# Performance work log

Measured on AMD Instinct MI355X. Metric: run time of the kernel, lower is better.

The kernel has to match this reference:

```python
import jax, jax.numpy as jnp
import numpy as np

EPS = 1e-12

def _layernorm(x, gamma, beta):
    m = jnp.mean(x, axis=-1, keepdims=True)
    v = jnp.mean((x - m) ** 2, axis=-1, keepdims=True)
    return (x - m) * jax.lax.rsqrt(v + EPS) * gamma + beta

def _gcn(x, node_emb, time_emb, W_pool, b_pool, gamma, beta):
    # x: [B, N, C]; node_emb: [N, D]; time_emb: [D]
    e = _layernorm(node_emb + time_emb[None, :], gamma, beta)          # [N, D] (dropout off: eval mode)
    A = jax.nn.softmax(e @ e.T, axis=1)                                 # [N, N] dynamic adjacency
    weights = jnp.einsum('nd,dkio->nkio', e, W_pool)                    # [N, 2, C, O] node-adaptive weights
    bias = e @ b_pool                                                   # [N, O]
    # supports = [I, A]; I support is identity -> x itself
    x_g = jnp.stack([x, jnp.einsum('nm,bmc->bnc', A, x)], axis=2)       # [B, N, 2, C]
    return jnp.einsum('bnki,nkio->bno', x_g, weights) + bias            # [B, N, O]

def setup_inputs() -> dict:
    key = jax.random.key(0)
    ks = jax.random.split(key, 16)
    B, N, Din, H, D = 64, 2048, 2, 64, 16
    C = Din + H
    inp = {
        'x': jax.random.normal(ks[0], (B, N, Din), jnp.float32),
        'state': jax.random.normal(ks[1], (B, N, H), jnp.float32),
        'node_embeddings': jax.random.normal(ks[2], (N, D), jnp.float32),
        'time_embeddings': jax.random.normal(ks[3], (D,), jnp.float32),
    }
    for i, g in enumerate(['z', 'r', 'u']):
        inp[f'W_{g}'] = jax.random.normal(ks[4 + 2 * i], (D, 2, C, H), jnp.float32) * 0.02
        inp[f'b_{g}'] = jax.random.normal(ks[5 + 2 * i], (D, H), jnp.float32) * 0.02
        inp[f'gamma_{g}'] = jnp.ones((D,), jnp.float32)
        inp[f'beta_{g}'] = jnp.zeros((D,), jnp.float32)
    return inp

def reference(x, state, node_embeddings, time_embeddings,
              W_z, b_z, gamma_z, beta_z,
              W_r, b_r, gamma_r, beta_r,
              W_u, b_u, gamma_u, beta_u):
    xs = jnp.concatenate([x, state], axis=-1)                           # [B, N, Din+H]
    z = jax.nn.sigmoid(_gcn(xs, node_embeddings, time_embeddings, W_z, b_z, gamma_z, beta_z))
    r = jax.nn.sigmoid(_gcn(xs, node_embeddings, time_embeddings, W_r, b_r, gamma_r, beta_r))
    cand = jnp.concatenate([x, z * state], axis=-1)
    hc = jnp.tanh(_gcn(cand, node_embeddings, time_embeddings, W_u, b_u, gamma_u, beta_u))
    return r * state + (1.0 - r) * hc
```

## Files before the change

kernel.cpp:

```cpp
#include <hip/hip_runtime.h>
#include <hip/hip_bf16.h>
#include <math.h>


typedef __attribute__((ext_vector_type(4))) float f4;
typedef __attribute__((ext_vector_type(8))) short s8;

#define B_   64
#define N_   2048
#define DIN  2
#define H_   64
#define D_   16
#define C_   66
#define KI   132
#define KIP  160
#define CB   4224

#define GLD16(gp, lp) __builtin_amdgcn_global_load_lds((const __attribute__((address_space(1))) void*)(gp), (__attribute__((address_space(3))) void*)(lp), 16, 0, 0)

static __device__ __forceinline__ ushort f2bf(float v) {
  __hip_bfloat16 h = __float2bfloat16(v);
  return *(ushort*)&h;
}
static __device__ __forceinline__ float bf2f(ushort u) {
  __hip_bfloat16 h = *(__hip_bfloat16*)&u;
  return __bfloat162float(h);
}
static __device__ __forceinline__ uint packbf(float a, float b) {
  return ((uint)f2bf(b) << 16) | f2bf(a);
}

__global__ void k_e(const float* __restrict__ node, const float* __restrict__ timee,
                    const float* __restrict__ g0, const float* __restrict__ b0,
                    const float* __restrict__ g1, const float* __restrict__ b1,
                    const float* __restrict__ g2, const float* __restrict__ b2,
                    float* __restrict__ e, ushort* __restrict__ ebf) {
  int n = blockIdx.x * blockDim.x + threadIdx.x;
  if (n >= N_) return;
  float v[D_]; float m = 0.f;
  #pragma unroll
  for (int d = 0; d < D_; ++d) { v[d] = node[n * D_ + d] + timee[d]; m += v[d]; }
  m *= (1.0f / D_);
  float var = 0.f;
  #pragma unroll
  for (int d = 0; d < D_; ++d) { float t = v[d] - m; var += t * t; }
  var *= (1.0f / D_);
  float r = rsqrtf(var + 1e-12f);
  float y[D_];
  #pragma unroll
  for (int d = 0; d < D_; ++d) y[d] = (v[d] - m) * r;
  const float* gs[3] = {g0, g1, g2};
  const float* bs[3] = {b0, b1, b2};
  #pragma unroll
  for (int g = 0; g < 3; ++g) {
    #pragma unroll
    for (int d = 0; d < D_; d += 2) {
      float o0 = y[d] * gs[g][d] + bs[g][d];
      float o1 = y[d + 1] * gs[g][d + 1] + bs[g][d + 1];
      e[g * N_ * D_ + n * D_ + d] = o0;
      e[g * N_ * D_ + n * D_ + d + 1] = o1;
      *(uint*)&ebf[g * N_ * D_ + n * D_ + d] = packbf(o0, o1);
    }
  }
}

__global__ __launch_bounds__(256)
void k_attn(const ushort* __restrict__ ebf, __hip_bfloat16* __restrict__ A) {
  __shared__ __align__(16) ushort eb[N_ * D_];
  __shared__ float red[4][16];
  const int t = threadIdx.x;
  const ushort* eg = ebf + (size_t)blockIdx.z * (N_ * D_);
  {
    const uint4* src = (const uint4*)eg;
    uint4* dst = (uint4*)eb;
    #pragma unroll
    for (int i = 0; i < 16; ++i) dst[i * 256 + t] = src[i * 256 + t];
  }
  __syncthreads();
  const int lane = t & 63, w = t >> 6;
  const int l15 = lane & 15, q = lane >> 4;
  const int r0 = blockIdx.x * 16;
  s8 rf = {0, 0, 0, 0, 0, 0, 0, 0};
  if (q < 2) rf = *(const s8*)&eb[(r0 + l15) * D_ + q * 8];
  const int c0 = w * 512;
  f4 acc[32];
  #pragma unroll
  for (int tl = 0; tl < 32; ++tl) {
    s8 cf = {0, 0, 0, 0, 0, 0, 0, 0};
    if (q < 2) cf = *(const s8*)&eb[(c0 + tl * 16 + l15) * D_ + q * 8];
    acc[tl] = __builtin_amdgcn_mfma_f32_16x16x32_bf16(cf, rf, (f4)0.0f, 0, 0, 0);
  }
  float m = acc[0][0];
  #pragma unroll
  for (int tl = 0; tl < 32; ++tl) {
    #pragma unroll
    for (int rg = 0; rg < 4; ++rg) m = fmaxf(m, acc[tl][rg]);
  }
  m = fmaxf(m, __shfl_xor(m, 16, 64));
  m = fmaxf(m, __shfl_xor(m, 32, 64));
  if (lane < 16) red[w][l15] = m;
  __syncthreads();
  const float gm = fmaxf(fmaxf(red[0][l15], red[1][l15]), fmaxf(red[2][l15], red[3][l15]));
  __syncthreads();
  float ps = 0.f;
  #pragma unroll
  for (int tl = 0; tl < 32; ++tl) {
    #pragma unroll
    for (int rg = 0; rg < 4; ++rg) {
      float v = __expf(acc[tl][rg] - gm);
      acc[tl][rg] = v;
      ps += v;
    }
  }
  ps += __shfl_xor(ps, 16, 64);
  ps += __shfl_xor(ps, 32, 64);
  if (lane < 16) red[w][l15] = ps;
  __syncthreads();
  const float inv = 1.0f / (red[0][l15] + red[1][l15] + red[2][l15] + red[3][l15]);
  ushort* Ar = (ushort*)A + (size_t)blockIdx.z * ((size_t)N_ * N_) +
               (size_t)(r0 + l15) * N_ + c0 + q * 4;
  #pragma unroll
  for (int tl = 0; tl < 32; ++tl) {
    uint2 pk;
    pk.x = packbf(acc[tl][0] * inv, acc[tl][1] * inv);
    pk.y = packbf(acc[tl][2] * inv, acc[tl][3] * inv);
    *(uint2*)&Ar[tl * 16] = pk;
  }
}

template <int MODE>
__global__ __launch_bounds__(256)
void k_buildX(const float* __restrict__ x, const float* __restrict__ state,
              const __hip_bfloat16* __restrict__ zbuf, __hip_bfloat16* __restrict__ XT) {
  constexpr int LDM = 72;
  __shared__ __align__(16) ushort T[C_ * LDM];
  const int t = threadIdx.x;
  const int m0 = blockIdx.x * 64, b = blockIdx.y;
  const int m = t >> 2, hq = t & 3;
  {
    const float* sp = state + ((size_t)b * N_ + m0 + m) * H_ + hq * 16;
    float sv[16];
    #pragma unroll
    for (int i = 0; i < 16; i += 4) {
      float4 v = *(const float4*)(sp + i);
      sv[i] = v.x; sv[i + 1] = v.y; sv[i + 2] = v.z; sv[i + 3] = v.w;
    }
    if (MODE) {
      const ushort* zp = (const ushort*)zbuf + ((size_t)b * N_ + m0 + m) * H_ + hq * 16;
      uint4 z0 = *(const uint4*)&zp[0], z1 = *(const uint4*)&zp[8];
      uint zw[8] = {z0.x, z0.y, z0.z, z0.w, z1.x, z1.y, z1.z, z1.w};
      #pragma unroll
      for (int i = 0; i < 8; ++i) {
        sv[2 * i]     *= bf2f((ushort)(zw[i] & 0xffffu));
        sv[2 * i + 1] *= bf2f((ushort)(zw[i] >> 16));
      }
    }
    #pragma unroll
    for (int i = 0; i < 16; ++i) T[(DIN + hq * 16 + i) * LDM + m] = f2bf(sv[i]);
    if (t < 64) {
      const float2 xv = *(const float2*)&x[((size_t)b * N_ + m0 + t) * DIN];
      T[0 * LDM + t] = f2bf(xv.x);
      T[1 * LDM + t] = f2bf(xv.y);
    }
  }
  __syncthreads();
  {
    int r = t >> 2, ch = t & 3;
    ushort* dst = (ushort*)XT + (size_t)(b * C_ + r) * N_ + m0 + ch * 16;
    *(uint4*)&dst[0] = *(uint4*)&T[r * LDM + ch * 16];
    *(uint4*)&dst[8] = *(uint4*)&T[r * LDM + ch * 16 + 8];
    if (t < 8) {
      r = 64 + (t >> 2);
      ushort* dst2 = (ushort*)XT + (size_t)(b * C_ + r) * N_ + m0 + ch * 16;
      *(uint4*)&dst2[0] = *(uint4*)&T[r * LDM + ch * 16];
      *(uint4*)&dst2[8] = *(uint4*)&T[r * LDM + ch * 16 + 8];
    }
  }
}

__global__ __launch_bounds__(256)
void k_gemm(const __hip_bfloat16* __restrict__ Abase, size_t astride,
            const __hip_bfloat16* __restrict__ XT,
            __hip_bfloat16* __restrict__ Ybase, size_t ystride) {
  __shared__ __align__(16) ushort At[2][128 * 32];
  __shared__ __align__(16) ushort Xt[2][128 * 32];
  const int t = threadIdx.x;
  const int nwg = gridDim.x * gridDim.y * gridDim.z;
  const int orig = blockIdx.x + gridDim.x * (blockIdx.y + gridDim.y * blockIdx.z);
  const int chunk = nwg >> 3;
  const int swz = (orig & 7) * chunk + (orig >> 3);
  const int bx = swz % gridDim.x;
  const int rest = swz / gridDim.x;
  const int by = rest % gridDim.y;
  const int bz = rest / gridDim.y;
  const int j0 = bx * 128, r0 = by * 128;
  const ushort* Ag = (const ushort*)Abase + (size_t)bz * astride;
  ushort* Y = (ushort*)Ybase + (size_t)bz * ystride;
  const int lane = t & 63, w = t >> 6;
  const int rowa = w * 32 + (lane >> 2);
  const int kc = (((lane & 3) ^ ((lane >> 3) & 3)) * 8);
  const ushort* pA0 = Ag + (size_t)(r0 + rowa) * N_ + kc;
  const ushort* pA1 = pA0 + 16 * N_;
  const ushort* pX0 = (const ushort*)XT + (size_t)(j0 + rowa) * N_ + kc;
  const ushort* pX1 = pX0 + 16 * N_;
  const int l15 = t & 15, q = (t >> 4) & 3;
  const int qs = (q ^ ((l15 >> 1) & 3)) * 8;
  const int wr = (w >> 1) * 64, wc = (w & 1) * 64;
  f4 acc[4][4];
  #pragma unroll
  for (int i = 0; i < 4; ++i)
    #pragma unroll
    for (int jj = 0; jj < 4; ++jj) acc[i][jj] = (f4)0.0f;
  GLD16(pA0, &At[0][(w * 32) * 32]);
  GLD16(pA1, &At[0][(w * 32 + 16) * 32]);
  GLD16(pX0, &Xt[0][(w * 32) * 32]);
  GLD16(pX1, &Xt[0][(w * 32 + 16) * 32]);
  pA0 += 32; pA1 += 32; pX0 += 32; pX1 += 32;
  int cur = 0;
  for (int k0 = 0; k0 < N_; k0 += 32) {
    if (k0 + 32 < N_) {
      const int nx = cur ^ 1;
      GLD16(pA0, &At[nx][(w * 32) * 32]);
      GLD16(pA1, &At[nx][(w * 32 + 16) * 32]);
      GLD16(pX0, &Xt[nx][(w * 32) * 32]);
      GLD16(pX1, &Xt[nx][(w * 32 + 16) * 32]);
      pA0 += 32; pA1 += 32; pX0 += 32; pX1 += 32;
      asm volatile("s_waitcnt vmcnt(4)" ::: "memory");
    } else {
      asm volatile("s_waitcnt vmcnt(0)" ::: "memory");
    }
    __builtin_amdgcn_s_barrier();
    __builtin_amdgcn_sched_barrier(0);
    s8 af[4], bfr[4];
    #pragma unroll
    for (int mi = 0; mi < 4; ++mi)
      af[mi] = *(const s8*)&At[cur][(wr + mi * 16 + l15) * 32 + qs];
    #pragma unroll
    for (int ni = 0; ni < 4; ++ni)
      bfr[ni] = *(const s8*)&Xt[cur][(wc + ni * 16 + l15) * 32 + qs];
    __builtin_amdgcn_s_setprio(1);
    #pragma unroll
    for (int mi = 0; mi < 4; ++mi)
      #pragma unroll
      for (int ni = 0; ni < 4; ++ni)
        acc[mi][ni] = __builtin_amdgcn_mfma_f32_16x16x32_bf16(af[mi], bfr[ni], acc[mi][ni], 0, 0, 0);
    __builtin_amdgcn_s_setprio(0);
    __builtin_amdgcn_s_barrier();
    cur ^= 1;
  }
  #pragma unroll
  for (int mi = 0; mi < 4; ++mi) {
    int rr = r0 + wr + mi * 16 + q * 4;
    #pragma unroll
    for (int ni = 0; ni < 4; ++ni) {
      int cc = j0 + wc + ni * 16 + l15;
      #pragma unroll
      for (int rg = 0; rg < 4; ++rg)
        Y[(size_t)(rr + rg) * CB + cc] = f2bf(acc[mi][ni][rg]);
    }
  }
}

__global__ __launch_bounds__(256)
void k_wmat(const float* __restrict__ eg, const float* __restrict__ Wp, ushort* __restrict__ Wm) {
  constexpr int TRS = 36;
  __shared__ float Wl[16 * 8 * 64];
  __shared__ ushort Tr[8 * 64 * TRS];
  const int t = threadIdx.x;
  const int n0 = blockIdx.x * 8;
  const int y = blockIdx.y;
  const int o = t & 63, w = t >> 6;
  const int ng = w & 1, krh = (w >> 1) * 4;
  float er[4][16];
  #pragma unroll
  for (int j = 0; j < 4; ++j) {
    const float* ep = eg + (size_t)(n0 + ng * 4 + j) * D_;
    #pragma unroll
    for (int d = 0; d < D_; d += 4) {
      float4 v = *(const float4*)(ep + d);
      er[j][d] = v.x; er[j][d + 1] = v.y; er[j][d + 2] = v.z; er[j][d + 3] = v.w;
    }
  }
  const int ngroups = (y == 3) ? 2 : 1;
  for (int g = 0; g < ngroups; ++g) {
    const int kic0 = y * 4 + g * 4;
    for (int kk = 0; kk < 4; ++kk) {
      const int kic = kic0 + kk;
      __syncthreads();
      #pragma unroll
      for (int it = 0; it < 8; ++it) {
        int f = it * 256 + t;
        int d = f >> 7, rem = f & 127, kr = rem >> 4, o4 = rem & 15;
        int ki = kic * 8 + kr;
        float4 v;
        if (ki < KI) v = *(const float4*)&Wp[((size_t)d * KI + ki) * 64 + o4 * 4];
        else { v.x = 0.f; v.y = 0.f; v.z = 0.f; v.w = 0.f; }
        *(float4*)&Wl[f * 4] = v;
      }
      __syncthreads();
      float a[4][4];
      #pragma unroll
      for (int j = 0; j < 4; ++j)
        #pragma unroll
        for (int k = 0; k < 4; ++k) a[j][k] = 0.f;
      for (int d = 0; d < D_; ++d) {
        float w4[4];
        #pragma unroll
        for (int k = 0; k < 4; ++k) w4[k] = Wl[(d * 8 + krh + k) * 64 + o];
        #pragma unroll
        for (int j = 0; j < 4; ++j)
          #pragma unroll
          for (int k = 0; k < 4; ++k) a[j][k] = fmaf(er[j][d], w4[k], a[j][k]);
      }
      #pragma unroll
      for (int j = 0; j < 4; ++j) {
        ushort* tr = &Tr[((ng * 4 + j) * 64 + o) * TRS + kk * 8 + krh];
        *(uint*)&tr[0] = packbf(a[j][0], a[j][1]);
        *(uint*)&tr[2] = packbf(a[j][2], a[j][3]);
      }
    }
    __syncthreads();
    const int k0 = kic0 * 8;
    #pragma unroll
    for (int p = 0; p < 8; ++p) {
      int u = p * 256 + t;
      int nl = u >> 8, oo = (u >> 2) & 63, qq = u & 3;
      const ushort* tr = &Tr[(nl * 64 + oo) * TRS + qq * 8];
      uint2 lo = *(const uint2*)&tr[0];
      uint2 hi = *(const uint2*)&tr[4];
      uint4 vv; vv.x = lo.x; vv.y = lo.y; vv.z = hi.x; vv.w = hi.y;
      *(uint4*)&Wm[((size_t)(n0 + nl) * 64 + oo) * KIP + k0 + qq * 8] = vv;
    }
  }
}

template <int MODE>
__global__ __launch_bounds__(256)
void k_einsum(const float* __restrict__ e, const ushort* __restrict__ Wm, const float* __restrict__ bp,
              const __hip_bfloat16* __restrict__ Y,
              const float* __restrict__ x, const float* __restrict__ state,
              const __hip_bfloat16* __restrict__ zbuf, const __hip_bfloat16* __restrict__ rbuf,
              void* __restrict__ outp) {
  constexpr int LDK = 168;
  constexpr int LDR = 72;
  __shared__ __align__(16) ushort xg[64 * LDK];
  __shared__ __align__(16) ushort res[64 * LDR];
  __shared__ float el[D_];
  __shared__ float bl[64];
  const int n = blockIdx.x, t = threadIdx.x;
  if (t < D_) el[t] = e[n * D_ + t];
  __syncthreads();
  if (t < 64) {
    float s = 0.f;
    #pragma unroll
    for (int d = 0; d < D_; ++d) s += el[d] * bp[d * 64 + t];
    bl[t] = s;
  }
  {
    const int b = t >> 2, j = t & 3;
    const size_t bn = (size_t)b * N_ + n;
    float sv[16];
    const float* sp = state + bn * 64 + j * 16;
    #pragma unroll
    for (int i = 0; i < 16; i += 4) {
      float4 v = *(const float4*)(sp + i);
      sv[i] = v.x; sv[i + 1] = v.y; sv[i + 2] = v.z; sv[i + 3] = v.w;
    }
    if (MODE) {
      const ushort* zp = (const ushort*)zbuf + bn * 64 + j * 16;
      uint4 z0 = *(const uint4*)&zp[0], z1 = *(const uint4*)&zp[8];
      uint zw[8] = {z0.x, z0.y, z0.z, z0.w, z1.x, z1.y, z1.z, z1.w};
      #pragma unroll
      for (int i = 0; i < 8; ++i) {
        sv[2 * i]     *= bf2f((ushort)(zw[i] & 0xffffu));
        sv[2 * i + 1] *= bf2f((ushort)(zw[i] >> 16));
      }
    }
    ushort* xr = &xg[b * LDK + 2 + j * 16];
    #pragma unroll
    for (int i = 0; i < 16; i += 2) {
      uint pk = packbf(sv[i], sv[i + 1]);
      *(uint*)&xr[i] = pk;
    }
    const ushort* yp = (const ushort*)Y + (size_t)n * CB + b * C_ + j * 16;
    uint* xy = (uint*)&xg[b * LDK + 66 + j * 16];
    #pragma unroll
    for (int i = 0; i < 8; ++i) xy[i] = *(const uint*)&yp[2 * i];
    if (j == 0) *(uint*)&xg[b * LDK + 130] = *(const uint*)&yp[64];
    if (t < 64) {
      const float* xp = x + ((size_t)t * N_ + n) * DIN;
      uint pk = packbf(xp[0], xp[1]);
      *(uint*)&xg[t * LDK] = pk;
    }
    ushort* pg = &xg[b * LDK + 132 + j * 7];
    #pragma unroll
    for (int i = 0; i < 7; ++i) pg[i] = 0;
  }
  __syncthreads();
  const int l15 = t & 15, q = (t >> 4) & 3, w = t >> 6;
  const int wm = (w >> 1) * 32, wn = (w & 1) * 32;
  const ushort* Wn = Wm + (size_t)n * (64 * KIP);
  f4 acc[2][2];
  acc[0][0] = acc[0][1] = acc[1][0] = acc[1][1] = (f4)0.0f;
  #pragma unroll
  for (int kk = 0; kk < KIP; kk += 32) {
    s8 af[2], bfr[2];
    #pragma unroll
    for (int mi = 0; mi < 2; ++mi) af[mi] = *(const s8*)&xg[(wm + mi * 16 + l15) * LDK + kk + q * 8];
    #pragma unroll
    for (int ni = 0; ni < 2; ++ni) bfr[ni] = *(const s8*)(Wn + (size_t)(wn + ni * 16 + l15) * KIP + kk + q * 8);
    #pragma unroll
    for (int mi = 0; mi < 2; ++mi)
      #pragma unroll
      for (int ni = 0; ni < 2; ++ni)
        acc[mi][ni] = __builtin_amdgcn_mfma_f32_16x16x32_bf16(af[mi], bfr[ni], acc[mi][ni], 0, 0, 0);
  }
  {
    float bl0 = bl[wn + l15], bl1 = bl[wn + 16 + l15];
    #pragma unroll
    for (int mi = 0; mi < 2; ++mi)
      #pragma unroll
      for (int ni = 0; ni < 2; ++ni) {
        float bb = ni ? bl1 : bl0;
        #pragma unroll
        for (int rg = 0; rg < 4; ++rg) {
          float v = acc[mi][ni][rg] + bb;
          float a;
          if (MODE == 0) a = 1.0f / (1.0f + __expf(-v));
          else           a = 1.0f - 2.0f / (__expf(2.0f * v) + 1.0f);
          res[(wm + mi * 16 + q * 4 + rg) * LDR + (wn + ni * 16 + l15)] = f2bf(a);
        }
      }
  }
  __syncthreads();
  {
    const int b = t >> 2, j = t & 3;
    const size_t gb = ((size_t)b * N_ + n) * 64 + j * 16;
    const ushort* rr = &res[b * LDR + j * 16];
    if (MODE == 0) {
      uint4 v0 = *(const uint4*)&rr[0];
      uint4 v1 = *(const uint4*)&rr[8];
      *(uint4*)((ushort*)outp + gb) = v0;
      *(uint4*)((ushort*)outp + gb + 8) = v1;
    } else {
      float* ob = (float*)outp;
      const float* stp = state + gb;
      const ushort* rp = (const ushort*)rbuf + gb;
      uint4 r0 = *(const uint4*)&rp[0], r1 = *(const uint4*)&rp[8];
      uint rw[8] = {r0.x, r0.y, r0.z, r0.w, r1.x, r1.y, r1.z, r1.w};
      #pragma unroll
      for (int i = 0; i < 16; i += 4) {
        float4 st = *(const float4*)(stp + i);
        float4 ov;
        float rv0 = bf2f((ushort)(rw[i / 2] & 0xffffu));
        float rv1 = bf2f((ushort)(rw[i / 2] >> 16));
        float rv2 = bf2f((ushort)(rw[i / 2 + 1] & 0xffffu));
        float rv3 = bf2f((ushort)(rw[i / 2 + 1] >> 16));
        ov.x = rv0 * st.x + (1.0f - rv0) * bf2f(rr[i]);
        ov.y = rv1 * st.y + (1.0f - rv1) * bf2f(rr[i + 1]);
        ov.z = rv2 * st.z + (1.0f - rv2) * bf2f(rr[i + 2]);
        ov.w = rv3 * st.w + (1.0f - rv3) * bf2f(rr[i + 3]);
        *(float4*)(ob + gb + i) = ov;
      }
    }
  }
}

extern "C" void kernel_launch(void* const* d_in, const int* in_sizes, int n_in,
                              void* d_out, int out_size, void* d_ws, size_t ws_size,
                              hipStream_t stream) {
  const float* x     = (const float*)d_in[0];
  const float* state = (const float*)d_in[1];
  const float* node  = (const float*)d_in[2];
  const float* timee = (const float*)d_in[3];
  const float* W_z = (const float*)d_in[4];
  const float* b_z = (const float*)d_in[5];
  const float* g_z = (const float*)d_in[6];
  const float* be_z = (const float*)d_in[7];
  const float* W_r = (const float*)d_in[8];
  const float* b_r = (const float*)d_in[9];
  const float* g_r = (const float*)d_in[10];
  const float* be_r = (const float*)d_in[11];
  const float* W_u = (const float*)d_in[12];
  const float* b_u = (const float*)d_in[13];
  const float* g_u = (const float*)d_in[14];
  const float* be_u = (const float*)d_in[15];

  constexpr size_t NN = (size_t)N_ * N_;
  constexpr size_t ND = (size_t)N_ * D_;
  char* ws = (char*)d_ws;
  float*           e  = (float*)(ws);
  __hip_bfloat16*  A  = (__hip_bfloat16*)(ws + 393216);
  __hip_bfloat16*  XT = (__hip_bfloat16*)(ws + 25559040);
  __hip_bfloat16*  Y  = (__hip_bfloat16*)(ws + 42860544);
  __hip_bfloat16*  zb = (__hip_bfloat16*)(ws + 60162048);
  __hip_bfloat16*  rb = (__hip_bfloat16*)(ws + 76939264);
  ushort*          ebf = (ushort*)(ws + 93716480);
  ushort*          Wm = (ushort*)(ws + 93716480);
  __hip_bfloat16*  Yr = (__hip_bfloat16*)(ws + 135659520);
  const size_t YRD = ((size_t)135659520 - 42860544) / 2;
  const bool big = ws_size >= (size_t)152961024;

  float* out = (float*)d_out;

  k_e<<<8, 256, 0, stream>>>(node, timee, g_z, be_z, g_r, be_r, g_u, be_u, e, ebf);
  k_attn<<<dim3(N_ / 16, 1, 3), 256, 0, stream>>>(ebf, A);
  k_buildX<0><<<dim3(32, 64), 256, 0, stream>>>(x, state, nullptr, XT);

  dim3 ggrid1(CB / 128, N_ / 128, 1);
  dim3 ggrid2(CB / 128, N_ / 128, 2);
  dim3 wgrid(N_ / 8, 4);

  if (big) {
    k_wmat<<<wgrid, 256, 0, stream>>>(e + 0 * ND, W_z, Wm);
    k_gemm<<<ggrid2, 256, 0, stream>>>(A, NN, XT, Y, YRD);
    k_einsum<0><<<N_, 256, 0, stream>>>(e + 0 * ND, Wm, b_z, Y, x, state, nullptr, nullptr, (void*)zb);
    k_wmat<<<wgrid, 256, 0, stream>>>(e + 1 * ND, W_r, Wm);
    k_einsum<0><<<N_, 256, 0, stream>>>(e + 1 * ND, Wm, b_r, Yr, x, state, nullptr, nullptr, (void*)rb);
  } else {
    k_wmat<<<wgrid, 256, 0, stream>>>(e + 0 * ND, W_z, Wm);
    k_gemm<<<ggrid1, 256, 0, stream>>>(A, 0, XT, Y, 0);
    k_einsum<0><<<N_, 256, 0, stream>>>(e + 0 * ND, Wm, b_z, Y, x, state, nullptr, nullptr, (void*)zb);
    k_wmat<<<wgrid, 256, 0, stream>>>(e + 1 * ND, W_r, Wm);
    k_gemm<<<ggrid1, 256, 0, stream>>>(A + NN, 0, XT, Y, 0);
    k_einsum<0><<<N_, 256, 0, stream>>>(e + 1 * ND, Wm, b_r, Y, x, state, nullptr, nullptr, (void*)rb);
  }
  k_buildX<1><<<dim3(32, 64), 256, 0, stream>>>(x, state, zb, XT);
  k_wmat<<<wgrid, 256, 0, stream>>>(e + 2 * ND, W_u, Wm);
  k_gemm<<<ggrid1, 256, 0, stream>>>(A + 2 * NN, 0, XT, Y, 0);
  k_einsum<1><<<N_, 256, 0, stream>>>(e + 2 * ND, Wm, b_u, Y, x, state, zb, rb, (void*)out);
}
```

Baseline: 486.3 us.

## Load GEMM X operand directly into registers, bypassing LDS, with one barrier per step

In k_gemm the X (B-side) tile is no longer staged through shared memory. Each wave loads its MFMA fragments straight from global memory into registers, double-buffered across two unrolled steps. The A tile still goes through LDS, but the trailing barrier of each step is gone, and launch bounds now request 3 waves per SIMD. The aim is to cut LDS footprint, LDS write and read traffic, and barrier overhead. In exchange, pairs of waves redundantly fetch the same X data from global/L2, and the loads use uncached-latency register paths that the compiler must wait on.

```diff
diff --git a/kernel.cpp b/kernel.cpp
--- a/kernel.cpp
+++ b/kernel.cpp
@@ -178,12 +178,11 @@
   }
 }
 
-__global__ __launch_bounds__(256)
+__global__ __launch_bounds__(256, 3)
 void k_gemm(const __hip_bfloat16* __restrict__ Abase, size_t astride,
             const __hip_bfloat16* __restrict__ XT,
             __hip_bfloat16* __restrict__ Ybase, size_t ystride) {
   __shared__ __align__(16) ushort At[2][128 * 32];
-  __shared__ __align__(16) ushort Xt[2][128 * 32];
   const int t = threadIdx.x;
   const int nwg = gridDim.x * gridDim.y * gridDim.z;
   const int orig = blockIdx.x + gridDim.x * (blockIdx.y + gridDim.y * blockIdx.z);
@@ -201,11 +200,13 @@
   const int kc = (((lane & 3) ^ ((lane >> 3) & 3)) * 8);
   const ushort* pA0 = Ag + (size_t)(r0 + rowa) * N_ + kc;
   const ushort* pA1 = pA0 + 16 * N_;
-  const ushort* pX0 = (const ushort*)XT + (size_t)(j0 + rowa) * N_ + kc;
-  const ushort* pX1 = pX0 + 16 * N_;
   const int l15 = t & 15, q = (t >> 4) & 3;
   const int qs = (q ^ ((l15 >> 1) & 3)) * 8;
   const int wr = (w >> 1) * 64, wc = (w & 1) * 64;
+  const ushort* pX0 = (const ushort*)XT + (size_t)(j0 + wc + l15) * N_ + q * 8;
+  const ushort* pX1 = pX0 + (size_t)16 * N_;
+  const ushort* pX2 = pX0 + (size_t)32 * N_;
+  const ushort* pX3 = pX0 + (size_t)48 * N_;
   f4 acc[4][4];
   #pragma unroll
   for (int i = 0; i < 4; ++i)
@@ -213,41 +214,54 @@
     for (int jj = 0; jj < 4; ++jj) acc[i][jj] = (f4)0.0f;
   GLD16(pA0, &At[0][(w * 32) * 32]);
   GLD16(pA1, &At[0][(w * 32 + 16) * 32]);
-  GLD16(pX0, &Xt[0][(w * 32) * 32]);
-  GLD16(pX1, &Xt[0][(w * 32 + 16) * 32]);
-  pA0 += 32; pA1 += 32; pX0 += 32; pX1 += 32;
-  int cur = 0;
-  for (int k0 = 0; k0 < N_; k0 += 32) {
-    if (k0 + 32 < N_) {
-      const int nx = cur ^ 1;
-      GLD16(pA0, &At[nx][(w * 32) * 32]);
-      GLD16(pA1, &At[nx][(w * 32 + 16) * 32]);
-      GLD16(pX0, &Xt[nx][(w * 32) * 32]);
-      GLD16(pX1, &Xt[nx][(w * 32 + 16) * 32]);
-      pA0 += 32; pA1 += 32; pX0 += 32; pX1 += 32;
-      asm volatile("s_waitcnt vmcnt(4)" ::: "memory");
-    } else {
-      asm volatile("s_waitcnt vmcnt(0)" ::: "memory");
-    }
-    __builtin_amdgcn_s_barrier();
-    __builtin_amdgcn_sched_barrier(0);
-    s8 af[4], bfr[4];
-    #pragma unroll
-    for (int mi = 0; mi < 4; ++mi)
-      af[mi] = *(const s8*)&At[cur][(wr + mi * 16 + l15) * 32 + qs];
-    #pragma unroll
-    for (int ni = 0; ni < 4; ++ni)
-      bfr[ni] = *(const s8*)&Xt[cur][(wc + ni * 16 + l15) * 32 + qs];
-    __builtin_amdgcn_s_setprio(1);
-    #pragma unroll
-    for (int mi = 0; mi < 4; ++mi)
-      #pragma unroll
-      for (int ni = 0; ni < 4; ++ni)
-        acc[mi][ni] = __builtin_amdgcn_mfma_f32_16x16x32_bf16(af[mi], bfr[ni], acc[mi][ni], 0, 0, 0);
-    __builtin_amdgcn_s_setprio(0);
-    __builtin_amdgcn_s_barrier();
-    cur ^= 1;
-  }
+  pA0 += 32; pA1 += 32;
+  s8 xa0 = *(const s8*)pX0, xa1 = *(const s8*)pX1;
+  s8 xa2 = *(const s8*)pX2, xa3 = *(const s8*)pX3;
+  pX0 += 32; pX1 += 32; pX2 += 32; pX3 += 32;
+  s8 xb0 = {0,0,0,0,0,0,0,0}, xb1 = xb0, xb2 = xb0, xb3 = xb0;
+
+#define GSTEP(CUR, NXT, XC0, XC1, XC2, XC3, XN0, XN1, XN2, XN3, LAST)           \
+  {                                                                             \
+    asm volatile("s_waitcnt vmcnt(4)" ::: "memory");                            \
+    __builtin_amdgcn_s_barrier();                                               \
+    __builtin_amdgcn_sched_barrier(0);                                          \
+    if (!(LAST)) {                                                              \
+      GLD16(pA0, &At[NXT][(w * 32) * 32]);                                      \
+      GLD16(pA1, &At[NXT][(w * 32 + 16) * 32]);                                 \
+      pA0 += 32; pA1 += 32;                                                     \
+      XN0 = *(const s8*)pX0; XN1 = *(const s8*)pX1;                             \
+      XN2 = *(const s8*)pX2; XN3 = *(const s8*)pX3;                             \
+      pX0 += 32; pX1 += 32; pX2 += 32; pX3 += 32;                               \
+    }                                                                           \
+    s8 af0 = *(const s8*)&At[CUR][(wr + 0 * 16 + l15) * 32 + qs];               \
+    s8 af1 = *(const s8*)&At[CUR][(wr + 1 * 16 + l15) * 32 + qs];               \
+    s8 af2 = *(const s8*)&At[CUR][(wr + 2 * 16 + l15) * 32 + qs];               \
+    s8 af3 = *(const s8*)&At[CUR][(wr + 3 * 16 + l15) * 32 + qs];               \
+    __builtin_amdgcn_s_setprio(1);                                              \
+    acc[0][0] = __builtin_amdgcn_mfma_f32_16x16x32_bf16(af0, XC0, acc[0][0], 0, 0, 0); \
+    acc[0][1] = __builtin_amdgcn_mfma_f32_16x16x32_bf16(af0, XC1, acc[0][1], 0, 0, 0); \
+    acc[0][2] = __builtin_amdgcn_mfma_f32_16x16x32_bf16(af0, XC2, acc[0][2], 0, 0, 0); \
+    acc[0][3] = __builtin_amdgcn_mfma_f32_16x16x32_bf16(af0, XC3, acc[0][3], 0, 0, 0); \
+    acc[1][0] = __builtin_amdgcn_mfma_f32_16x16x32_bf16(af1, XC0, acc[1][0], 0, 0, 0); \
+    acc[1][1] = __builtin_amdgcn_mfma_f32_16x16x32_bf16(af1, XC1, acc[1][1], 0, 0, 0); \
+    acc[1][2] = __builtin_amdgcn_mfma_f32_16x16x32_bf16(af1, XC2, acc[1][2], 0, 0, 0); \
+    acc[1][3] = __builtin_amdgcn_mfma_f32_16x16x32_bf16(af1, XC3, acc[1][3], 0, 0, 0); \
+    acc[2][0] = __builtin_amdgcn_mfma_f32_16x16x32_bf16(af2, XC0, acc[2][0], 0, 0, 0); \
+    acc[2][1] = __builtin_amdgcn_mfma_f32_16x16x32_bf16(af2, XC1, acc[2][1], 0, 0, 0); \
+    acc[2][2] = __builtin_amdgcn_mfma_f32_16x16x32_bf16(af2, XC2, acc[2][2], 0, 0, 0); \
+    acc[2][3] = __builtin_amdgcn_mfma_f32_16x16x32_bf16(af2, XC3, acc[2][3], 0, 0, 0); \
+    acc[3][0] = __builtin_amdgcn_mfma_f32_16x16x32_bf16(af3, XC0, acc[3][0], 0, 0, 0); \
+    acc[3][1] = __builtin_amdgcn_mfma_f32_16x16x32_bf16(af3, XC1, acc[3][1], 0, 0, 0); \
+    acc[3][2] = __builtin_amdgcn_mfma_f32_16x16x32_bf16(af3, XC2, acc[3][2], 0, 0, 0); \
+    acc[3][3] = __builtin_amdgcn_mfma_f32_16x16x32_bf16(af3, XC3, acc[3][3], 0, 0, 0); \
+    __builtin_amdgcn_s_setprio(0);                                              \
+  }
+
+  for (int it = 0; it < 32; ++it) {
+    GSTEP(0, 1, xa0, xa1, xa2, xa3, xb0, xb1, xb2, xb3, 0)
+    GSTEP(1, 0, xb0, xb1, xb2, xb3, xa0, xa1, xa2, xa3, (it == 31))
+  }
+#undef GSTEP
   #pragma unroll
   for (int mi = 0; mi < 4; ++mi) {
     int rr = r0 + wr + mi * 16 + q * 4;
```

Measured after the change: 617.1 us. 26.9% more time.
